# Optimization experiments

Measured on AMD Instinct MI355X. Metric: run time of the kernel, lower is better.

The kernel has to match this reference:

```python
import jax, jax.numpy as jnp
import numpy as np

NEG_SLOPE = 0.2


def gcn_conv(x, W, b, src, dst, w, n):
    # x: [N, F_in], W: [F_in, F_out], edge (src -> dst) with weight w.
    xw = x @ W  # [N, F_out]
    # add self-loops with weight 1 (PyG GCNConv default)
    loop = jnp.arange(n)
    src_f = jnp.concatenate([src, loop])
    dst_f = jnp.concatenate([dst, loop])
    w_f = jnp.concatenate([w, jnp.ones((n,), dtype=w.dtype)])
    # symmetric normalization: deg computed on destination
    deg = jax.ops.segment_sum(w_f, dst_f, num_segments=n)
    dinv = jnp.where(deg > 0, jax.lax.rsqrt(deg), 0.0)
    norm = dinv[src_f] * w_f * dinv[dst_f]  # [E+N]
    msg = xw[src_f] * norm[:, None]          # [E+N, F_out]
    out = jax.ops.segment_sum(msg, dst_f, num_segments=n)
    return out + b


def setup_inputs() -> dict:
    key = jax.random.key(0)
    k1, k2, k3, k4, k5 = jax.random.split(key, 5)
    N, E, F_in, F_hid, F_out = 100000, 3200000, 128, 128, 64
    x = jax.random.normal(k1, (N, F_in), dtype=jnp.float32)
    edge_index = jax.random.randint(k2, (2, E), 0, N, dtype=jnp.int64)
    edge_weight = jax.random.uniform(k3, (E,), dtype=jnp.float32)
    s1 = 1.0 / np.sqrt(F_in)
    s2 = 1.0 / np.sqrt(F_hid)
    W1 = jax.random.uniform(k4, (F_in, F_hid), minval=-s1, maxval=s1, dtype=jnp.float32)
    b1 = jnp.zeros((F_hid,), dtype=jnp.float32)
    W2 = jax.random.uniform(k5, (F_hid, F_out), minval=-s2, maxval=s2, dtype=jnp.float32)
    b2 = jnp.zeros((F_out,), dtype=jnp.float32)
    return {"x": x, "edge_index": edge_index, "edge_weight": edge_weight,
            "W1": W1, "b1": b1, "W2": W2, "b2": b2}


def reference(x, edge_index, edge_weight, W1, b1, W2, b2):
    n = x.shape[0]
    src, dst = edge_index[0], edge_index[1]
    h = gcn_conv(x, W1, b1, src, dst, edge_weight, n)
    h = jax.nn.leaky_relu(h, NEG_SLOPE)
    # dropout is identity in eval mode
    h = gcn_conv(h, W2, b2, src, dst, edge_weight, n)
    return jax.nn.log_softmax(h, axis=1)
```

## Files before the change

### kernel.cpp

```cpp
#include <hip/hip_runtime.h>
#include <cstdint>
#include <cstddef>

#define NEG_SLOPE 0.2f
#define CH 8192
#define CAP 6144
#define BN 128

typedef short v8s __attribute__((ext_vector_type(8)));
typedef float v4f __attribute__((ext_vector_type(4)));

static __device__ __forceinline__ float b2f(unsigned short u) {
  return __uint_as_float((unsigned)u << 16);
}
static __device__ __forceinline__ unsigned short f2b(float f) {
  unsigned u = __float_as_uint(f);
  return (unsigned short)((u + 0x7FFFu + ((u >> 16) & 1u)) >> 16);
}
static __device__ __forceinline__ ushort4 f2b4(float4 v) {
  ushort4 r; r.x = f2b(v.x); r.y = f2b(v.y); r.z = f2b(v.z); r.w = f2b(v.w); return r;
}
static __device__ __forceinline__ int pk(float lo, float hi) {
  return (int)((unsigned)f2b(lo) | ((unsigned)f2b(hi) << 16));
}

static __device__ __forceinline__ int edge_at(const void* ei, int is32, long long pos) {
  return is32 ? ((const int*)ei)[pos] : (int)(((const long long*)ei)[pos]);
}

__global__ void k_init(unsigned* gcur, int* flag, int nb) {
  int i = blockIdx.x * blockDim.x + threadIdx.x;
  if (i < nb) gcur[i] = 0u;
  if (i == 0) flag[0] = 0;
}

__global__ void k_detect(const int* ei32, int* flag, long long n32) {
  int i = blockIdx.x * blockDim.x + threadIdx.x;
  long long idx = 2LL * i + 1;
  if (idx < 2048 && idx < n32) {
    if (ei32[idx] != 0) atomicOr(flag, 1);
  }
}

__global__ __launch_bounds__(256) void k_part(const void* __restrict__ ei, const float* __restrict__ ew,
                                              const int* __restrict__ flag,
                                              int2* __restrict__ recs, unsigned* __restrict__ gcur,
                                              int E, int nb) {
  __shared__ unsigned hist[1024];
  __shared__ unsigned bas[1024];
  __shared__ unsigned erank[CH];
  int tid = threadIdx.x;
  for (int i = tid; i < nb; i += 256) hist[i] = 0u;
  __syncthreads();
  int is32 = *flag;
  int c0 = blockIdx.x * CH;
#pragma unroll
  for (int j = 0; j < CH / 256; ++j) {
    int idx = c0 + j * 256 + tid;
    if (idx < E) {
      int d = edge_at(ei, is32, (long long)E + idx);
      int b = d >> 7, dl = d & (BN - 1);
      unsigned r = atomicAdd(&hist[b], 1u);
      erank[j * 256 + tid] = ((unsigned)b << 20) | ((unsigned)dl << 13) | r;
    }
  }
  __syncthreads();
  for (int i = tid; i < nb; i += 256) {
    unsigned c = hist[i];
    bas[i] = c ? atomicAdd(&gcur[i], c) : 0u;
  }
  __syncthreads();
#pragma unroll
  for (int j = 0; j < CH / 256; ++j) {
    int idx = c0 + j * 256 + tid;
    if (idx < E) {
      unsigned er = erank[j * 256 + tid];
      int b = (int)(er >> 20);
      int dl = (int)((er >> 13) & (BN - 1));
      unsigned p = bas[b] + (er & 8191u);
      if (p < CAP) {
        int s = edge_at(ei, is32, idx);
        float w = ew[idx];
        recs[(size_t)b * CAP + p] = make_int2(s | (dl << 17), __float_as_int(w));
      }
    }
  }
}

__global__ __launch_bounds__(256) void k_deg(const int2* __restrict__ recs, const unsigned* __restrict__ gcur,
                                             float* __restrict__ dinv, int2* __restrict__ rp2, int N) {
  __shared__ float degL[BN];
  __shared__ unsigned cntL[BN], pref[BN];
  int b = blockIdx.x, tid = threadIdx.x;
  if (tid < BN) { degL[tid] = 1.0f; cntL[tid] = 0u; }
  __syncthreads();
  int cnt = min((int)gcur[b], CAP);
  const int2* rb = recs + (size_t)b * CAP;
  for (int e = tid; e < cnt; e += 256) {
    int2 rc = rb[e];
    int dl = (rc.x >> 17) & (BN - 1);
    atomicAdd(&degL[dl], __int_as_float(rc.y));
    atomicAdd(&cntL[dl], 1u);
  }
  __syncthreads();
  if (tid < BN) pref[tid] = cntL[tid];
  __syncthreads();
  for (int d = 1; d < BN; d <<= 1) {
    unsigned v = 0u;
    if (tid < BN && tid >= d) v = pref[tid - d];
    __syncthreads();
    if (tid < BN) pref[tid] += v;
    __syncthreads();
  }
  int gnode = b * BN + tid;
  if (tid < BN && gnode < N) {
    dinv[gnode] = rsqrtf(degL[tid]);
    unsigned st = pref[tid] - cntL[tid];
    rp2[gnode] = make_int2(b * CAP + (int)st, b * CAP + (int)pref[tid]);
  }
}

__global__ __launch_bounds__(256) void k_bin(const int2* __restrict__ recs, const unsigned* __restrict__ gcur,
                                             const float* __restrict__ dinv, const int2* __restrict__ rp2,
                                             int2* __restrict__ pairs, int N) {
  __shared__ unsigned baseL[BN], cnt2[BN];
  int b = blockIdx.x, tid = threadIdx.x;
  if (tid < BN) {
    int gnode = b * BN + tid;
    baseL[tid] = (gnode < N) ? (unsigned)(rp2[gnode].x - b * CAP) : 0u;
    cnt2[tid] = 0u;
  }
  __syncthreads();
  int cnt = min((int)gcur[b], CAP);
  const int2* rb = recs + (size_t)b * CAP;
  for (int e = tid; e < cnt; e += 256) {
    int2 rc = rb[e];
    int dl = (rc.x >> 17) & (BN - 1);
    int s = rc.x & 0x1FFFF;
    unsigned r = atomicAdd(&cnt2[dl], 1u);
    float nm = dinv[s] * __int_as_float(rc.y);
    pairs[(size_t)b * CAP + baseL[dl] + r] = make_int2(s, __float_as_int(nm));
  }
}

template <int FOUT, bool XBF>
__global__ __launch_bounds__(256) void k_gemmM(const void* __restrict__ Xv,
                                               const float* __restrict__ W,
                                               unsigned short* __restrict__ Y, int M) {
  constexpr int NI = FOUT / 64;
  __shared__ int4 XsV[128 * 16];
  int t = threadIdx.x;
  int wv = t >> 6, ln = t & 63;
  int row0 = blockIdx.x * 128;
  int lq = ln >> 4;
  int lr = ln & 15;

  v8s bfr[4][NI];
#pragma unroll
  for (int kst = 0; kst < 4; ++kst)
#pragma unroll
    for (int ni = 0; ni < NI; ++ni) {
      int col = wv * (16 * NI) + ni * 16 + lr;
#pragma unroll
      for (int j = 0; j < 8; ++j) {
        int k = kst * 32 + lq * 8 + j;
        bfr[kst][ni][j] = (short)f2b(W[k * FOUT + col]);
      }
    }

#pragma unroll
  for (int j = 0; j < 8; ++j) {
    int idx = j * 256 + t;
    int row = idx >> 4, u = idx & 15;
    int gr = row0 + row;
    int4 out;
    if (gr < M) {
      if constexpr (XBF) {
        out = ((const int4*)Xv)[(size_t)gr * 16 + u];
      } else {
        float4 a = ((const float4*)Xv)[(size_t)gr * 32 + u * 2];
        float4 bq = ((const float4*)Xv)[(size_t)gr * 32 + u * 2 + 1];
        out = make_int4(pk(a.x, a.y), pk(a.z, a.w), pk(bq.x, bq.y), pk(bq.z, bq.w));
      }
    } else {
      out = make_int4(0, 0, 0, 0);
    }
    XsV[row * 16 + (u ^ (row & 7))] = out;
  }
  __syncthreads();

  v4f acc[8][NI];
#pragma unroll
  for (int mi = 0; mi < 8; ++mi)
#pragma unroll
    for (int ni = 0; ni < NI; ++ni) acc[mi][ni] = (v4f)(0.0f);

#pragma unroll
  for (int kst = 0; kst < 4; ++kst) {
    int u = kst * 4 + lq;
#pragma unroll
    for (int mi = 0; mi < 8; ++mi) {
      int row = mi * 16 + lr;
      v8s a = *(const v8s*)&XsV[row * 16 + (u ^ (row & 7))];
#pragma unroll
      for (int ni = 0; ni < NI; ++ni)
        acc[mi][ni] = __builtin_amdgcn_mfma_f32_16x16x32_bf16(a, bfr[kst][ni], acc[mi][ni], 0, 0, 0);
    }
  }

#pragma unroll
  for (int mi = 0; mi < 8; ++mi) {
#pragma unroll
    for (int ni = 0; ni < NI; ++ni) {
      int col = wv * (16 * NI) + ni * 16 + lr;
#pragma unroll
      for (int r = 0; r < 4; ++r) {
        int grow = row0 + mi * 16 + lq * 4 + r;
        if (grow < M) Y[(size_t)grow * FOUT + col] = f2b(acc[mi][ni][r]);
      }
    }
  }
}

__global__ __launch_bounds__(256) void k_agg1(const ushort4* __restrict__ xwb, const float* __restrict__ dinv,
                                              const int2* __restrict__ rp2, const int2* __restrict__ pairs,
                                              const float* __restrict__ b1,
                                              ushort4* __restrict__ hb, int n) {
  int wid = threadIdx.x >> 6;
  int lane = threadIdx.x & 63;
  int node = blockIdx.x * 4 + wid;
  if (node >= n) return;
  int half = lane >> 5;
  int fo = lane & 31;
  float di = dinv[node];
  float4 acc = make_float4(0.f, 0.f, 0.f, 0.f);
  int2 rr = rp2[node];
  int e = rr.x, e1 = rr.y;
  for (; e + 16 <= e1; e += 16) {
    int2 p[8];
#pragma unroll
    for (int j = 0; j < 8; ++j) p[j] = pairs[e + 2 * j + half];
    ushort4 v[8];
#pragma unroll
    for (int j = 0; j < 8; ++j) v[j] = xwb[(size_t)p[j].x * 32 + fo];
#pragma unroll
    for (int j = 0; j < 8; ++j) {
      float nm = __int_as_float(p[j].y);
      acc.x = fmaf(b2f(v[j].x), nm, acc.x);
      acc.y = fmaf(b2f(v[j].y), nm, acc.y);
      acc.z = fmaf(b2f(v[j].z), nm, acc.z);
      acc.w = fmaf(b2f(v[j].w), nm, acc.w);
    }
  }
  for (; e < e1; e += 2) {
    int ee = e + half;
    if (ee < e1) {
      int2 p = pairs[ee];
      ushort4 v = xwb[(size_t)p.x * 32 + fo];
      float nm = __int_as_float(p.y);
      acc.x = fmaf(b2f(v.x), nm, acc.x);
      acc.y = fmaf(b2f(v.y), nm, acc.y);
      acc.z = fmaf(b2f(v.z), nm, acc.z);
      acc.w = fmaf(b2f(v.w), nm, acc.w);
    }
  }
  acc.x += __shfl_xor(acc.x, 32, 64);
  acc.y += __shfl_xor(acc.y, 32, 64);
  acc.z += __shfl_xor(acc.z, 32, 64);
  acc.w += __shfl_xor(acc.w, 32, 64);
  ushort4 sv = xwb[(size_t)node * 32 + fo];
  acc.x = fmaf(b2f(sv.x), di, acc.x);
  acc.y = fmaf(b2f(sv.y), di, acc.y);
  acc.z = fmaf(b2f(sv.z), di, acc.z);
  acc.w = fmaf(b2f(sv.w), di, acc.w);
  float4 b = ((const float4*)b1)[fo];
  acc.x = fmaf(acc.x, di, b.x);
  acc.y = fmaf(acc.y, di, b.y);
  acc.z = fmaf(acc.z, di, b.z);
  acc.w = fmaf(acc.w, di, b.w);
  acc.x = acc.x > 0.f ? acc.x : NEG_SLOPE * acc.x;
  acc.y = acc.y > 0.f ? acc.y : NEG_SLOPE * acc.y;
  acc.z = acc.z > 0.f ? acc.z : NEG_SLOPE * acc.z;
  acc.w = acc.w > 0.f ? acc.w : NEG_SLOPE * acc.w;
  if (half == 0) hb[(size_t)node * 32 + fo] = f2b4(acc);
}

__global__ __launch_bounds__(256) void k_agg2(const ushort4* __restrict__ hwb, const float* __restrict__ dinv,
                                              const int2* __restrict__ rp2, const int2* __restrict__ pairs,
                                              const float* __restrict__ b2,
                                              float* __restrict__ out, int n) {
  int wid = threadIdx.x >> 6;
  int lane = threadIdx.x & 63;
  int node = blockIdx.x * 4 + wid;
  if (node >= n) return;
  int q = lane >> 4;
  int fo = lane & 15;
  float di = dinv[node];
  float4 acc = make_float4(0.f, 0.f, 0.f, 0.f);
  int2 rr = rp2[node];
  int e = rr.x, e1 = rr.y;
  for (; e + 32 <= e1; e += 32) {
    int2 p[8];
#pragma unroll
    for (int j = 0; j < 8; ++j) p[j] = pairs[e + 4 * j + q];
    ushort4 v[8];
#pragma unroll
    for (int j = 0; j < 8; ++j) v[j] = hwb[(size_t)p[j].x * 16 + fo];
#pragma unroll
    for (int j = 0; j < 8; ++j) {
      float nm = __int_as_float(p[j].y);
      acc.x = fmaf(b2f(v[j].x), nm, acc.x);
      acc.y = fmaf(b2f(v[j].y), nm, acc.y);
      acc.z = fmaf(b2f(v[j].z), nm, acc.z);
      acc.w = fmaf(b2f(v[j].w), nm, acc.w);
    }
  }
  for (; e < e1; e += 4) {
    int ee = e + q;
    if (ee < e1) {
      int2 p = pairs[ee];
      ushort4 v = hwb[(size_t)p.x * 16 + fo];
      float nm = __int_as_float(p.y);
      acc.x = fmaf(b2f(v.x), nm, acc.x);
      acc.y = fmaf(b2f(v.y), nm, acc.y);
      acc.z = fmaf(b2f(v.z), nm, acc.z);
      acc.w = fmaf(b2f(v.w), nm, acc.w);
    }
  }
#pragma unroll
  for (int d = 32; d >= 16; d >>= 1) {
    acc.x += __shfl_xor(acc.x, d, 64);
    acc.y += __shfl_xor(acc.y, d, 64);
    acc.z += __shfl_xor(acc.z, d, 64);
    acc.w += __shfl_xor(acc.w, d, 64);
  }
  ushort4 sv = hwb[(size_t)node * 16 + fo];
  acc.x = fmaf(b2f(sv.x), di, acc.x);
  acc.y = fmaf(b2f(sv.y), di, acc.y);
  acc.z = fmaf(b2f(sv.z), di, acc.z);
  acc.w = fmaf(b2f(sv.w), di, acc.w);
  float4 b = ((const float4*)b2)[fo];
  acc.x = fmaf(acc.x, di, b.x);
  acc.y = fmaf(acc.y, di, b.y);
  acc.z = fmaf(acc.z, di, b.z);
  acc.w = fmaf(acc.w, di, b.w);
  float m = fmaxf(fmaxf(acc.x, acc.y), fmaxf(acc.z, acc.w));
#pragma unroll
  for (int d = 8; d >= 1; d >>= 1) m = fmaxf(m, __shfl_xor(m, d, 64));
  float s = expf(acc.x - m) + expf(acc.y - m) + expf(acc.z - m) + expf(acc.w - m);
#pragma unroll
  for (int d = 8; d >= 1; d >>= 1) s += __shfl_xor(s, d, 64);
  float lse = m + logf(s);
  if (q == 0) {
    float4 o = make_float4(acc.x - lse, acc.y - lse, acc.z - lse, acc.w - lse);
    ((float4*)out)[(size_t)node * 16 + fo] = o;
  }
}

extern "C" void kernel_launch(void* const* d_in, const int* in_sizes, int n_in,
                              void* d_out, int out_size, void* d_ws, size_t ws_size,
                              hipStream_t stream) {
  const float* x  = (const float*)d_in[0];
  const void*  ei = d_in[1];
  const float* ew = (const float*)d_in[2];
  const float* W1 = (const float*)d_in[3];
  const float* b1 = (const float*)d_in[4];
  const float* W2 = (const float*)d_in[5];
  const float* b2 = (const float*)d_in[6];
  float* out = (float*)d_out;

  const int Fh = in_sizes[4];
  const int Fi = in_sizes[3] / Fh;
  const int N  = in_sizes[0] / Fi;
  const int E  = in_sizes[2];
  const int NB = (N + BN - 1) / BN;

  char* ws = (char*)d_ws;
  size_t o = 0;
  auto alloc = [&](size_t bytes) { size_t r = o; o += (bytes + 255) & ~(size_t)255; return r; };
  ushort4* xwb  = (ushort4*)(ws + alloc((size_t)N * 128 * 2));
  ushort4* hb   = (ushort4*)(ws + alloc((size_t)N * 128 * 2));
  int2*    prs  = (int2*)   (ws + alloc((size_t)NB * CAP * 8));
  float*   dinv = (float*)  (ws + alloc((size_t)N * 4));
  int2*    rp2  = (int2*)   (ws + alloc((size_t)(N + BN) * 8));
  unsigned* gcur= (unsigned*)(ws + alloc((size_t)NB * 4));
  int*     flag = (int*)    (ws + alloc(4));
  (void)ws_size;
  int2* recs_tmp = (int2*)xwb;

  const int tb = 256;
  const int nchunks = (E + CH - 1) / CH;

  hipLaunchKernelGGL(k_init,   dim3((NB + tb - 1) / tb), dim3(tb), 0, stream, gcur, flag, NB);
  hipLaunchKernelGGL(k_detect, dim3(1), dim3(1024), 0, stream, (const int*)ei, flag, 2LL * E);
  hipLaunchKernelGGL(k_part,   dim3(nchunks), dim3(tb), 0, stream, ei, ew, flag, recs_tmp, gcur, E, NB);
  hipLaunchKernelGGL(k_deg,    dim3(NB), dim3(tb), 0, stream, recs_tmp, gcur, dinv, rp2, N);
  hipLaunchKernelGGL(k_bin,    dim3(NB), dim3(tb), 0, stream, recs_tmp, gcur, dinv, rp2, prs, N);

  hipLaunchKernelGGL((k_gemmM<128, false>), dim3((N + 127) / 128), dim3(tb), 0, stream,
                     (const void*)x, W1, (unsigned short*)xwb, N);
  hipLaunchKernelGGL(k_agg1,   dim3((N + 3) / 4), dim3(tb), 0, stream, xwb, dinv, rp2, prs, b1, hb, N);
  hipLaunchKernelGGL((k_gemmM<64, true>),   dim3((N + 127) / 128), dim3(tb), 0, stream,
                     (const void*)hb, W2, (unsigned short*)xwb, N);
  hipLaunchKernelGGL(k_agg2,   dim3((N + 3) / 4), dim3(tb), 0, stream, xwb, dinv, rp2, prs, b2, out, N);
}
```

Baseline: 353.3 us.

## Fuse edge partitioning with first GEMM in one heterogeneous launch

Merges the edge-partition kernel and the layer-1 X·W1 GEMM into a single launch where the first blocks partition edges and the remaining blocks run the GEMM. The two independent stages can then overlap on the GPU. Index-width detection moves into each partition block, which removes the separate init-flag and detect launches. Records now get their own workspace buffer instead of aliasing xwb, which costs extra memory, and the merged kernel's shared-memory and register footprint may reduce occupancy for both halves.

```diff
diff --git a/kernel.cpp b/kernel.cpp
--- a/kernel.cpp
+++ b/kernel.cpp
@@ -28,60 +28,125 @@
   return is32 ? ((const int*)ei)[pos] : (int)(((const long long*)ei)[pos]);
 }
 
-__global__ void k_init(unsigned* gcur, int* flag, int nb) {
+__global__ void k_init(unsigned* gcur, int nb) {
   int i = blockIdx.x * blockDim.x + threadIdx.x;
   if (i < nb) gcur[i] = 0u;
-  if (i == 0) flag[0] = 0;
-}
-
-__global__ void k_detect(const int* ei32, int* flag, long long n32) {
-  int i = blockIdx.x * blockDim.x + threadIdx.x;
-  long long idx = 2LL * i + 1;
-  if (idx < 2048 && idx < n32) {
-    if (ei32[idx] != 0) atomicOr(flag, 1);
-  }
-}
-
-__global__ __launch_bounds__(256) void k_part(const void* __restrict__ ei, const float* __restrict__ ew,
-                                              const int* __restrict__ flag,
-                                              int2* __restrict__ recs, unsigned* __restrict__ gcur,
-                                              int E, int nb) {
-  __shared__ unsigned hist[1024];
-  __shared__ unsigned bas[1024];
-  __shared__ unsigned erank[CH];
+}
+
+__global__ __launch_bounds__(256) void k_partgemm(const void* __restrict__ ei, const float* __restrict__ ew,
+                                                  int2* __restrict__ recs, unsigned* __restrict__ gcur,
+                                                  int E, int nb, int nchunks,
+                                                  const float* __restrict__ X, const float* __restrict__ W,
+                                                  unsigned short* __restrict__ Y, int M) {
+  __shared__ int4 sm4[2560];
+  __shared__ int is32sh;
   int tid = threadIdx.x;
-  for (int i = tid; i < nb; i += 256) hist[i] = 0u;
-  __syncthreads();
-  int is32 = *flag;
-  int c0 = blockIdx.x * CH;
-#pragma unroll
-  for (int j = 0; j < CH / 256; ++j) {
-    int idx = c0 + j * 256 + tid;
-    if (idx < E) {
-      int d = edge_at(ei, is32, (long long)E + idx);
-      int b = d >> 7, dl = d & (BN - 1);
-      unsigned r = atomicAdd(&hist[b], 1u);
-      erank[j * 256 + tid] = ((unsigned)b << 20) | ((unsigned)dl << 13) | r;
-    }
-  }
-  __syncthreads();
-  for (int i = tid; i < nb; i += 256) {
-    unsigned c = hist[i];
-    bas[i] = c ? atomicAdd(&gcur[i], c) : 0u;
-  }
-  __syncthreads();
-#pragma unroll
-  for (int j = 0; j < CH / 256; ++j) {
-    int idx = c0 + j * 256 + tid;
-    if (idx < E) {
-      unsigned er = erank[j * 256 + tid];
-      int b = (int)(er >> 20);
-      int dl = (int)((er >> 13) & (BN - 1));
-      unsigned p = bas[b] + (er & 8191u);
-      if (p < CAP) {
-        int s = edge_at(ei, is32, idx);
-        float w = ew[idx];
-        recs[(size_t)b * CAP + p] = make_int2(s | (dl << 17), __float_as_int(w));
+
+  if (blockIdx.x < nchunks) {
+    unsigned* hist  = (unsigned*)sm4;
+    unsigned* bas   = (unsigned*)sm4 + 1024;
+    unsigned* erank = (unsigned*)sm4 + 2048;
+    if (tid == 0) is32sh = 0;
+    for (int i = tid; i < nb; i += 256) hist[i] = 0u;
+    __syncthreads();
+    if (((const int*)ei)[2 * tid + 1] != 0) atomicOr(&is32sh, 1);
+    __syncthreads();
+    int is32 = is32sh;
+    int c0 = blockIdx.x * CH;
+#pragma unroll
+    for (int j = 0; j < CH / 256; ++j) {
+      int idx = c0 + j * 256 + tid;
+      if (idx < E) {
+        int d = edge_at(ei, is32, (long long)E + idx);
+        int b = d >> 7, dl = d & (BN - 1);
+        unsigned r = atomicAdd(&hist[b], 1u);
+        erank[j * 256 + tid] = ((unsigned)b << 20) | ((unsigned)dl << 13) | r;
+      }
+    }
+    __syncthreads();
+    for (int i = tid; i < nb; i += 256) {
+      unsigned c = hist[i];
+      bas[i] = c ? atomicAdd(&gcur[i], c) : 0u;
+    }
+    __syncthreads();
+#pragma unroll
+    for (int j = 0; j < CH / 256; ++j) {
+      int idx = c0 + j * 256 + tid;
+      if (idx < E) {
+        unsigned er = erank[j * 256 + tid];
+        int b = (int)(er >> 20);
+        int dl = (int)((er >> 13) & (BN - 1));
+        unsigned p = bas[b] + (er & 8191u);
+        if (p < CAP) {
+          int s = edge_at(ei, is32, idx);
+          float w = ew[idx];
+          recs[(size_t)b * CAP + p] = make_int2(s | (dl << 17), __float_as_int(w));
+        }
+      }
+    }
+  } else {
+    int4* XsV = sm4;
+    int wv = tid >> 6, ln = tid & 63;
+    int row0 = (blockIdx.x - nchunks) * 128;
+    int lq = ln >> 4, lr = ln & 15;
+
+    v8s bfr[4][2];
+#pragma unroll
+    for (int kst = 0; kst < 4; ++kst)
+#pragma unroll
+      for (int ni = 0; ni < 2; ++ni) {
+        int col = wv * 32 + ni * 16 + lr;
+#pragma unroll
+        for (int j = 0; j < 8; ++j) {
+          int k = kst * 32 + lq * 8 + j;
+          bfr[kst][ni][j] = (short)f2b(W[k * 128 + col]);
+        }
+      }
+
+#pragma unroll
+    for (int j = 0; j < 8; ++j) {
+      int idx = j * 256 + tid;
+      int row = idx >> 4, u = idx & 15;
+      int gr = row0 + row;
+      int4 out = make_int4(0, 0, 0, 0);
+      if (gr < M) {
+        float4 a  = ((const float4*)X)[(size_t)gr * 32 + u * 2];
+        float4 bq = ((const float4*)X)[(size_t)gr * 32 + u * 2 + 1];
+        out = make_int4(pk(a.x, a.y), pk(a.z, a.w), pk(bq.x, bq.y), pk(bq.z, bq.w));
+      }
+      XsV[row * 16 + (u ^ (row & 7))] = out;
+    }
+    __syncthreads();
+
+    v4f acc[8][2];
+#pragma unroll
+    for (int mi = 0; mi < 8; ++mi)
+#pragma unroll
+      for (int ni = 0; ni < 2; ++ni) acc[mi][ni] = (v4f)(0.0f);
+
+#pragma unroll
+    for (int kst = 0; kst < 4; ++kst) {
+      int u = kst * 4 + lq;
+#pragma unroll
+      for (int mi = 0; mi < 8; ++mi) {
+        int row = mi * 16 + lr;
+        v8s a = *(const v8s*)&XsV[row * 16 + (u ^ (row & 7))];
+#pragma unroll
+        for (int ni = 0; ni < 2; ++ni)
+          acc[mi][ni] = __builtin_amdgcn_mfma_f32_16x16x32_bf16(a, bfr[kst][ni], acc[mi][ni], 0, 0, 0);
+      }
+    }
+
+#pragma unroll
+    for (int mi = 0; mi < 8; ++mi) {
+#pragma unroll
+      for (int ni = 0; ni < 2; ++ni) {
+        int col = wv * 32 + ni * 16 + lr;
+#pragma unroll
+        for (int r = 0; r < 4; ++r) {
+          int grow = row0 + mi * 16 + lq * 4 + r;
+          if (grow < M) Y[(size_t)grow * 128 + col] = f2b(acc[mi][ni][r]);
+        }
       }
     }
   }
@@ -143,7 +208,7 @@
   }
 }
 
-template <int FOUT, bool XBF>
+template <int FOUT>
 __global__ __launch_bounds__(256) void k_gemmM(const void* __restrict__ Xv,
                                                const float* __restrict__ W,
                                                unsigned short* __restrict__ Y, int M) {
@@ -152,8 +217,7 @@
   int t = threadIdx.x;
   int wv = t >> 6, ln = t & 63;
   int row0 = blockIdx.x * 128;
-  int lq = ln >> 4;
-  int lr = ln & 15;
+  int lq = ln >> 4, lr = ln & 15;
 
   v8s bfr[4][NI];
 #pragma unroll
@@ -173,18 +237,8 @@
     int idx = j * 256 + t;
     int row = idx >> 4, u = idx & 15;
     int gr = row0 + row;
-    int4 out;
-    if (gr < M) {
-      if constexpr (XBF) {
-        out = ((const int4*)Xv)[(size_t)gr * 16 + u];
-      } else {
-        float4 a = ((const float4*)Xv)[(size_t)gr * 32 + u * 2];
-        float4 bq = ((const float4*)Xv)[(size_t)gr * 32 + u * 2 + 1];
-        out = make_int4(pk(a.x, a.y), pk(a.z, a.w), pk(bq.x, bq.y), pk(bq.z, bq.w));
-      }
-    } else {
-      out = make_int4(0, 0, 0, 0);
-    }
+    int4 out = make_int4(0, 0, 0, 0);
+    if (gr < M) out = ((const int4*)Xv)[(size_t)gr * 16 + u];
     XsV[row * 16 + (u ^ (row & 7))] = out;
   }
   __syncthreads();
@@ -381,26 +435,25 @@
   ushort4* xwb  = (ushort4*)(ws + alloc((size_t)N * 128 * 2));
   ushort4* hb   = (ushort4*)(ws + alloc((size_t)N * 128 * 2));
   int2*    prs  = (int2*)   (ws + alloc((size_t)NB * CAP * 8));
+  int2*    recs = (int2*)   (ws + alloc((size_t)NB * CAP * 8));
   float*   dinv = (float*)  (ws + alloc((size_t)N * 4));
   int2*    rp2  = (int2*)   (ws + alloc((size_t)(N + BN) * 8));
   unsigned* gcur= (unsigned*)(ws + alloc((size_t)NB * 4));
-  int*     flag = (int*)    (ws + alloc(4));
   (void)ws_size;
-  int2* recs_tmp = (int2*)xwb;
 
   const int tb = 256;
   const int nchunks = (E + CH - 1) / CH;
-
-  hipLaunchKernelGGL(k_init,   dim3((NB + tb - 1) / tb), dim3(tb), 0, stream, gcur, flag, NB);
-  hipLaunchKernelGGL(k_detect, dim3(1), dim3(1024), 0, stream, (const int*)ei, flag, 2LL * E);
-  hipLaunchKernelGGL(k_part,   dim3(nchunks), dim3(tb), 0, stream, ei, ew, flag, recs_tmp, gcur, E, NB);
-  hipLaunchKernelGGL(k_deg,    dim3(NB), dim3(tb), 0, stream, recs_tmp, gcur, dinv, rp2, N);
-  hipLaunchKernelGGL(k_bin,    dim3(NB), dim3(tb), 0, stream, recs_tmp, gcur, dinv, rp2, prs, N);
-
-  hipLaunchKernelGGL((k_gemmM<128, false>), dim3((N + 127) / 128), dim3(tb), 0, stream,
-                     (const void*)x, W1, (unsigned short*)xwb, N);
-  hipLaunchKernelGGL(k_agg1,   dim3((N + 3) / 4), dim3(tb), 0, stream, xwb, dinv, rp2, prs, b1, hb, N);
-  hipLaunchKernelGGL((k_gemmM<64, true>),   dim3((N + 127) / 128), dim3(tb), 0, stream,
+  const int ngemm1 = (N + 127) / 128;
+
+  hipLaunchKernelGGL(k_init,     dim3((NB + tb - 1) / tb), dim3(tb), 0, stream, gcur, NB);
+  hipLaunchKernelGGL(k_partgemm, dim3(nchunks + ngemm1), dim3(tb), 0, stream,
+                     ei, ew, recs, gcur, E, NB, nchunks,
+                     x, W1, (unsigned short*)xwb, N);
+  hipLaunchKernelGGL(k_deg,      dim3(NB), dim3(tb), 0, stream, recs, gcur, dinv, rp2, N);
+  hipLaunchKernelGGL(k_bin,      dim3(NB), dim3(tb), 0, stream, recs, gcur, dinv, rp2, prs, N);
+
+  hipLaunchKernelGGL(k_agg1,     dim3((N + 3) / 4), dim3(tb), 0, stream, xwb, dinv, rp2, prs, b1, hb, N);
+  hipLaunchKernelGGL((k_gemmM<64>), dim3((N + 127) / 128), dim3(tb), 0, stream,
                      (const void*)hb, W2, (unsigned short*)xwb, N);
-  hipLaunchKernelGGL(k_agg2,   dim3((N + 3) / 4), dim3(tb), 0, stream, xwb, dinv, rp2, prs, b2, out, N);
-}
+  hipLaunchKernelGGL(k_agg2,     dim3((N + 3) / 4), dim3(tb), 0, stream, xwb, dinv, rp2, prs, b2, out, N);
+}
```

New measurement: 346.9 us, median of 2. Within noise of the previous version (-1.8%).
